# Optimization experiments

Measured on AMD Instinct MI355X. Metric: run time of the kernel, lower is better.

Reference implementation:

```python
import jax, jax.numpy as jnp
import numpy as np

B, N, D = 4, 4096, 512
E, H, TOPK = 4, 2048, 1
V_MAX, FEAT_CLAMP = 3.0, 10.0


def setup_inputs() -> dict:
    key = jax.random.key(0)
    ks = jax.random.split(key, 8)
    g = lambda k, shape, s: (jax.random.normal(k, shape, jnp.float32) * s)
    return {
        "x": g(ks[0], (B, N, D), 1.0),
        "gate_w": g(ks[1], (D, E), 0.02), "gate_b": jnp.zeros((E,), jnp.float32),
        "w1": g(ks[2], (E, D, H), 0.02), "b1": jnp.zeros((E, H), jnp.float32),
        "w2": g(ks[3], (E, H, D), 0.02), "b2": jnp.zeros((E, D), jnp.float32),
        "v_w": g(ks[4], (D,), 0.02), "v_b": jnp.zeros((), jnp.float32),
        "out_w": g(ks[5], (2, D), 0.02), "out_b": jnp.zeros((D,), jnp.float32),
        "bk_scale": jnp.asarray(1.0, jnp.float32),
    }


def _moe_ffn(x, gate_w, gate_b, w1, b1, w2, b2):
    # Sparse MoE FFN (eval mode, no dropout): top-k routing, softmax over top-k logits.
    logits = x @ gate_w + gate_b                       # (B,N,E)
    vals, idx = jax.lax.top_k(logits, TOPK)            # (B,N,K)
    wts = jax.nn.softmax(vals, axis=-1)                # (B,N,K); == 1.0 for top_k=1
    wfull = jnp.sum(jax.nn.one_hot(idx, E, dtype=x.dtype) * wts[..., None], axis=-2)  # (B,N,E)
    h = jax.nn.gelu(jnp.einsum('bnd,edh->benh', x, w1) + b1[None, :, None, :])
    y = jnp.einsum('benh,ehd->bend', h, w2) + b2[None, :, None, :]
    return jnp.einsum('bne,bend->bnd', wfull, y)


def _tridiag_green_diag(diag, sup, sub, z):
    # Diagonal of G = (T - z I)^{-1} for tridiagonal T via stable continuant ratios:
    #   L_i = theta_i/theta_{i-1},  R_i = phi_i/phi_{i+1},  G_ii = 1/(L_i + R_i - d_i)
    d = diag.astype(jnp.complex64) - z                 # (B,N)
    s = (sub * sup).astype(jnp.complex64)              # (B,N-1)
    dT = jnp.swapaxes(d, 0, 1)                         # (N,B)
    sT = jnp.swapaxes(s, 0, 1)                         # (N-1,B)

    def step(carry, inp):
        di, si = inp
        nxt = di - si / carry
        return nxt, nxt

    _, Lrest = jax.lax.scan(step, dT[0], (dT[1:], sT))
    L = jnp.concatenate([dT[:1], Lrest], axis=0)       # (N,B)
    _, Rrest = jax.lax.scan(step, dT[-1], (dT[:-1][::-1], sT[::-1]))
    R = jnp.concatenate([dT[-1:], Rrest], axis=0)[::-1]
    G = 1.0 / (L + R - dT)                             # (N,B)
    return jnp.swapaxes(G, 0, 1)                       # (B,N)


def reference(x, gate_w, gate_b, w1, b1, w2, b2, v_w, v_b, out_w, out_b, bk_scale):
    ffn_out = _moe_ffn(x, gate_w, gate_b, w1, b1, w2, b2)        # (B,N,D)
    v = jnp.clip(ffn_out @ v_w + v_b, -V_MAX, V_MAX)             # (B,N)
    he_diag = v - 2.0                                            # h0_diag_base = -2
    ones_off = jnp.ones((x.shape[0], x.shape[1] - 1), x.dtype)   # h0 sub/super = 1
    G = _tridiag_green_diag(he_diag, ones_off, ones_off, jnp.complex64(1j))
    feats = jnp.clip(jnp.stack([G.real, G.imag], axis=-1), -FEAT_CLAMP, FEAT_CLAMP)  # (B,N,2)
    spec = feats @ out_w + out_b                                 # (B,N,D)
    return ffn_out + bk_scale * spec
```

## Files before the change

### kernel.cpp

```cpp
#include <hip/hip_runtime.h>
#include <hip/hip_bf16.h>
#include <stdint.h>

#define TOK 16384
#define NSEQ 4096
#define BATCH 4
#define Dm 512
#define Em 4
#define Hm 2048

typedef __attribute__((ext_vector_type(4))) float f32x4;
typedef __attribute__((ext_vector_type(4))) unsigned int u32x4;

__device__ __forceinline__ unsigned short f2bf(float f) {
    union { float f; uint32_t u; } v; v.f = f;
    uint32_t u = v.u;
    uint32_t r = (u + 0x7FFFu + ((u >> 16) & 1u)) >> 16;
    return (unsigned short)r;
}

struct cpx { float re, im; };
__device__ __forceinline__ cpx cmul(cpx a, cpx b) { return { a.re*b.re - a.im*b.im, a.re*b.im + a.im*b.re }; }
__device__ __forceinline__ cpx csub(cpx a, cpx b) { return { a.re - b.re, a.im - b.im }; }
__device__ __forceinline__ cpx cadd(cpx a, cpx b) { return { a.re + b.re, a.im + b.im }; }
__device__ __forceinline__ cpx cdiv(cpx a, cpx b) {
    float inv = 1.0f / (b.re*b.re + b.im*b.im);
    return { (a.re*b.re + a.im*b.im)*inv, (a.im*b.re - a.re*b.im)*inv };
}

__device__ __forceinline__ void mfma_bf16(f32x4& acc, u32x4 a, u32x4 b) {
    asm("v_mfma_f32_16x16x32_bf16 %0, %1, %2, %0" : "+v"(acc) : "v"(a), "v"(b));
}

#define GLOAD_LDS16(g, l) \
    __builtin_amdgcn_global_load_lds((const __attribute__((address_space(1))) unsigned int*)(g), \
                                     (__attribute__((address_space(3))) unsigned int*)(l), 16, 0, 0)

__global__ __launch_bounds__(256) void gate_kernel(
    const float* __restrict__ x, const float* __restrict__ gate_w, const float* __restrict__ gate_b,
    unsigned short* __restrict__ xbf, int* __restrict__ expert_id)
{
    int wid = threadIdx.x >> 6, lane = threadIdx.x & 63;
    int t0 = (blockIdx.x * 4 + wid) * 8;

    const float4* gw4 = (const float4*)gate_w;
    float4 g[8];
#pragma unroll
    for (int j = 0; j < 8; j++) g[j] = gw4[lane * 8 + j];
    double gb0 = (double)gate_b[0], gb1 = (double)gate_b[1];
    double gb2 = (double)gate_b[2], gb3 = (double)gate_b[3];

    for (int tt = 0; tt < 8; tt++) {
        int t = t0 + tt;
        const float4* x4 = (const float4*)(x + (size_t)t * Dm);
        float4 xa = x4[lane * 2], xb = x4[lane * 2 + 1];

        uint4 pk;
        pk.x = (uint32_t)f2bf(xa.x) | ((uint32_t)f2bf(xa.y) << 16);
        pk.y = (uint32_t)f2bf(xa.z) | ((uint32_t)f2bf(xa.w) << 16);
        pk.z = (uint32_t)f2bf(xb.x) | ((uint32_t)f2bf(xb.y) << 16);
        pk.w = (uint32_t)f2bf(xb.z) | ((uint32_t)f2bf(xb.w) << 16);
        *(uint4*)(xbf + (size_t)t * Dm + lane * 8) = pk;

        float xv[8] = { xa.x, xa.y, xa.z, xa.w, xb.x, xb.y, xb.z, xb.w };
        double s0 = 0, s1 = 0, s2 = 0, s3 = 0;
#pragma unroll
        for (int j = 0; j < 8; j++) {
            s0 += (double)xv[j] * (double)g[j].x;
            s1 += (double)xv[j] * (double)g[j].y;
            s2 += (double)xv[j] * (double)g[j].z;
            s3 += (double)xv[j] * (double)g[j].w;
        }
#pragma unroll
        for (int off = 1; off < 64; off <<= 1) {
            s0 += __shfl_xor(s0, off);
            s1 += __shfl_xor(s1, off);
            s2 += __shfl_xor(s2, off);
            s3 += __shfl_xor(s3, off);
        }
        if (lane == 0) {
            double l0 = s0 + gb0, l1 = s1 + gb1, l2 = s2 + gb2, l3 = s3 + gb3;
            int e = 0; double best = l0;
            if (l1 > best) { best = l1; e = 1; }
            if (l2 > best) { best = l2; e = 2; }
            if (l3 > best) { best = l3; e = 3; }
            expert_id[t] = e;
        }
    }
}

__global__ __launch_bounds__(256) void transpose_cvt(
    const float* __restrict__ w1, const float* __restrict__ w2,
    unsigned short* __restrict__ w1t, unsigned short* __restrict__ w2t)
{
    int z = blockIdx.z;
    const float* src; unsigned short* dst; int R, C;
    if (z < 4) { src = w1 + (size_t)z * Dm * Hm; dst = w1t + (size_t)z * Hm * Dm; R = Dm; C = Hm; }
    else       { src = w2 + (size_t)(z - 4) * Hm * Dm; dst = w2t + (size_t)(z - 4) * Dm * Hm; R = Hm; C = Dm; }
    int c0 = blockIdx.x * 32, r0 = blockIdx.y * 32;
    if (c0 >= C || r0 >= R) return;
    __shared__ float tile[32][33];
    int tx = threadIdx.x & 31, ty = threadIdx.x >> 5;
#pragma unroll
    for (int i = 0; i < 4; i++)
        tile[ty + i * 8][tx] = src[(size_t)(r0 + ty + i * 8) * C + c0 + tx];
    __syncthreads();
#pragma unroll
    for (int i = 0; i < 4; i++)
        dst[(size_t)(c0 + ty + i * 8) * R + r0 + tx] = f2bf(tile[tx][ty + i * 8]);
}

__global__ __launch_bounds__(1024) void route_kernel(
    const int* __restrict__ expert_id, int* __restrict__ counts,
    int* __restrict__ offsets, int* __restrict__ rowmap)
{
    __shared__ int wcnt[16][4];
    __shared__ int woff[16][4];
    int wid = threadIdx.x >> 6, lane = threadIdx.x & 63;
    int base = wid * 1024;

    int myeid[16], myrank[16];
    int run0 = 0, run1 = 0, run2 = 0, run3 = 0;
#pragma unroll
    for (int s = 0; s < 16; s++) {
        int e = expert_id[base + s * 64 + lane];
        myeid[s] = e;
        unsigned long long b0 = __ballot(e & 1);
        unsigned long long b1 = __ballot(e & 2);
        unsigned long long m0 = (e & 1) ? b0 : ~b0;
        unsigned long long m1 = (e & 2) ? b1 : ~b1;
        unsigned long long same = m0 & m1;
        unsigned long long below = same & ((1ull << lane) - 1ull);
        int runh = (e == 0) ? run0 : (e == 1) ? run1 : (e == 2) ? run2 : run3;
        myrank[s] = runh + (int)__popcll(below);
        run0 += (int)__popcll(~b0 & ~b1);
        run1 += (int)__popcll(b0 & ~b1);
        run2 += (int)__popcll(~b0 & b1);
        run3 += (int)__popcll(b0 & b1);
    }
    if (lane == 0) {
        wcnt[wid][0] = run0; wcnt[wid][1] = run1; wcnt[wid][2] = run2; wcnt[wid][3] = run3;
    }
    __syncthreads();
    if (threadIdx.x == 0) {
        int t0 = 0, t1 = 0, t2 = 0, t3 = 0;
        for (int w = 0; w < 16; w++) {
            woff[w][0] = t0; woff[w][1] = t1; woff[w][2] = t2; woff[w][3] = t3;
            t0 += wcnt[w][0]; t1 += wcnt[w][1]; t2 += wcnt[w][2]; t3 += wcnt[w][3];
        }
        counts[0] = t0; counts[1] = t1; counts[2] = t2; counts[3] = t3;
        int o0 = 0, o1 = t0, o2 = t0 + t1, o3 = t0 + t1 + t2;
        offsets[0] = o0; offsets[1] = o1; offsets[2] = o2; offsets[3] = o3;
        for (int w = 0; w < 16; w++) {
            woff[w][0] += o0; woff[w][1] += o1; woff[w][2] += o2; woff[w][3] += o3;
        }
    }
    __syncthreads();
#pragma unroll
    for (int s = 0; s < 16; s++) {
        int e = myeid[s];
        rowmap[woff[wid][e] + myrank[s]] = base + s * 64 + lane;
    }
}

template<int KTOT, int NTOT, bool GATHER_A, bool GELU_EPI>
__global__ __launch_bounds__(256) void gemm_kernel(
    const unsigned short* __restrict__ A, const unsigned short* __restrict__ B,
    const float* __restrict__ bias,
    const int* __restrict__ counts, const int* __restrict__ offsets,
    const int* __restrict__ rowmap,
    unsigned short* __restrict__ Hout, float* __restrict__ Cout,
    const float* __restrict__ v_w, float* __restrict__ vpart)
{
    constexpr int NT = KTOT / 32;
    int e = blockIdx.z;
    int Me = counts[e];
    int mblk = blockIdx.y;
    if (mblk * 128 >= Me) return;
    int base = offsets[e];
    int nblk = blockIdx.x;
    int t = threadIdx.x, wid = t >> 6, lane = t & 63;

    __shared__ __align__(16) unsigned short As[3][128 * 32];
    __shared__ __align__(16) unsigned short Bs[3][128 * 32];

    const unsigned short* agp[2];
    const unsigned short* bgp[2];
#pragma unroll
    for (int c = 0; c < 2; c++) {
        int r = (c * 4 + wid) * 16 + (lane >> 2);
        int g = (lane & 3) ^ ((r >> 1) & 3);
        int mr = mblk * 128 + r; if (mr >= Me) mr = Me - 1;
        int arow = GATHER_A ? rowmap[base + mr] : (base + mr);
        agp[c] = A + (size_t)arow * KTOT + g * 8;
        int nr = nblk * 128 + r;
        bgp[c] = B + ((size_t)e * NTOT + nr) * (size_t)KTOT + g * 8;
    }

    int wm = wid >> 1, wn = wid & 1;
    int g = lane >> 4;
    int r0a = wm * 64 + (lane & 15);
    int r0b = wn * 64 + (lane & 15);
    int abase = r0a * 64 + ((g ^ ((r0a >> 1) & 3)) << 4);
    int bbase = r0b * 64 + ((g ^ ((r0b >> 1) & 3)) << 4);

    f32x4 acc[4][4] = {};

#define STAGE_T(bufi, kt) do { \
    _Pragma("unroll") \
    for (int c = 0; c < 2; c++) { \
        GLOAD_LDS16(agp[c] + (kt) * 32, &As[bufi][(c * 4 + wid) * 512]); \
        GLOAD_LDS16(bgp[c] + (kt) * 32, &Bs[bufi][(c * 4 + wid) * 512]); \
    } \
} while (0)

    STAGE_T(0, 0);
    STAGE_T(1, 1);
    int cur = 0;
    for (int kt = 0; kt < NT; ++kt) {
        int nb = cur + 2; if (nb >= 3) nb -= 3;
        if (kt + 2 < NT) {
            STAGE_T(nb, kt + 2);
            asm volatile("s_waitcnt vmcnt(8)" ::: "memory");
        } else if (kt + 1 < NT) {
            asm volatile("s_waitcnt vmcnt(4)" ::: "memory");
        } else {
            asm volatile("s_waitcnt vmcnt(0)" ::: "memory");
        }
        __builtin_amdgcn_s_barrier();

        const char* ab = (const char*)&As[cur][0];
        const char* bb = (const char*)&Bs[cur][0];
        u32x4 av[4], bv[4];
#pragma unroll
        for (int m = 0; m < 4; m++) av[m] = *(const u32x4*)(ab + abase + m * 1024);
#pragma unroll
        for (int n = 0; n < 4; n++) bv[n] = *(const u32x4*)(bb + bbase + n * 1024);
        __builtin_amdgcn_s_setprio(1);
#pragma unroll
        for (int m = 0; m < 4; m++)
#pragma unroll
            for (int n = 0; n < 4; n++)
                mfma_bf16(acc[m][n], av[m], bv[n]);
        __builtin_amdgcn_s_setprio(0);
        asm volatile("s_waitcnt lgkmcnt(0)" ::: "memory");
        __builtin_amdgcn_s_barrier();
        cur = (cur + 1 == 3) ? 0 : cur + 1;
    }
#undef STAGE_T

    float bb4[4], vw4[4];
#pragma unroll
    for (int n = 0; n < 4; n++) {
        int col = nblk * 128 + wn * 64 + n * 16 + (lane & 15);
        bb4[n] = bias[e * NTOT + col];
        if (!GELU_EPI) vw4[n] = v_w[col];
    }
#pragma unroll
    for (int m = 0; m < 4; m++) {
        int rbase = wm * 64 + m * 16 + ((lane >> 4) << 2);
#pragma unroll
        for (int j = 0; j < 4; j++) {
            int row = mblk * 128 + rbase + j;
            bool ok = row < Me;
            float p = 0.0f;
            int tok = 0;
            if (!GELU_EPI) tok = rowmap[base + (ok ? row : 0)];
#pragma unroll
            for (int n = 0; n < 4; n++) {
                int col = nblk * 128 + wn * 64 + n * 16 + (lane & 15);
                float v = acc[m][n][j] + bb4[n];
                if (GELU_EPI) {
                    if (ok) {
                        float u = 0.7978845608f * (v + 0.044715f * v * v * v);
                        float ex = __expf(2.0f * u);
                        float th = 1.0f - 2.0f / (ex + 1.0f);
                        float hv = 0.5f * v * (1.0f + th);
                        Hout[(size_t)(base + row) * NTOT + col] = f2bf(hv);
                    }
                } else {
                    if (ok) Cout[(size_t)tok * Dm + col] = v;
                    p += v * vw4[n];
                }
            }
            if (!GELU_EPI) {
                p += __shfl_xor(p, 1); p += __shfl_xor(p, 2);
                p += __shfl_xor(p, 4); p += __shfl_xor(p, 8);
                if (ok && (lane & 15) == 0) vpart[tok * 4 + nblk] = p;
            }
        }
    }
}

__global__ __launch_bounds__(256) void vdot2_kernel(
    const float4* __restrict__ vpart, const float* __restrict__ v_b, float* __restrict__ dre)
{
    int t = blockIdx.x * 256 + threadIdx.x;
    float4 p = vpart[t];
    float v = p.x + p.y + p.z + p.w + v_b[0];
    v = fminf(fmaxf(v, -3.0f), 3.0f);
    dre[t] = v - 2.0f;
}

#define SDI(i) ((i) + ((i) >> 6))
__global__ __launch_bounds__(64) void scan_kernel(
    const float* __restrict__ dre, float2* __restrict__ Lf, float2* __restrict__ Rb)
{
    int b = blockIdx.x >> 1, dir = blockIdx.x & 1;
    int lane = threadIdx.x;
    __shared__ float sd[4096 + 64];
    const float* src = dre + b * NSEQ;
    for (int i = lane; i < NSEQ; i += 64)
        sd[SDI(i)] = src[dir ? (NSEQ - 1 - i) : i];
    __syncthreads();

    cpx m00 = {1, 0}, m01 = {0, 0}, m10 = {0, 0}, m11 = {1, 0};
    int s0i = lane * 64;
#pragma unroll 4
    for (int j = 0; j < 64; j++) {
        cpx d = { sd[SDI(s0i + j)], -1.0f };
        cpx n00 = csub(cmul(d, m00), m10);
        cpx n01 = csub(cmul(d, m01), m11);
        m10 = m00; m11 = m01; m00 = n00; m01 = n01;
        if ((j & 15) == 15) {
            float mx = fmaxf(fmaxf(fmaxf(fabsf(m00.re), fabsf(m00.im)), fmaxf(fabsf(m01.re), fabsf(m01.im))),
                             fmaxf(fmaxf(fabsf(m10.re), fabsf(m10.im)), fmaxf(fabsf(m11.re), fabsf(m11.im))));
            float r = 1.0f / mx;
            m00.re *= r; m00.im *= r; m01.re *= r; m01.im *= r;
            m10.re *= r; m10.im *= r; m11.re *= r; m11.im *= r;
        }
    }

#pragma unroll
    for (int off = 1; off < 64; off <<= 1) {
        cpx q00, q01, q10, q11;
        q00.re = __shfl_up(m00.re, off); q00.im = __shfl_up(m00.im, off);
        q01.re = __shfl_up(m01.re, off); q01.im = __shfl_up(m01.im, off);
        q10.re = __shfl_up(m10.re, off); q10.im = __shfl_up(m10.im, off);
        q11.re = __shfl_up(m11.re, off); q11.im = __shfl_up(m11.im, off);
        if (lane >= off) {
            cpx r00 = cadd(cmul(m00, q00), cmul(m01, q10));
            cpx r01 = cadd(cmul(m00, q01), cmul(m01, q11));
            cpx r10 = cadd(cmul(m10, q00), cmul(m11, q10));
            cpx r11 = cadd(cmul(m10, q01), cmul(m11, q11));
            m00 = r00; m01 = r01; m10 = r10; m11 = r11;
            float mx = fmaxf(fmaxf(fmaxf(fabsf(m00.re), fabsf(m00.im)), fmaxf(fabsf(m01.re), fabsf(m01.im))),
                             fmaxf(fmaxf(fabsf(m10.re), fabsf(m10.im)), fmaxf(fabsf(m11.re), fabsf(m11.im))));
            float r = 1.0f / mx;
            m00.re *= r; m00.im *= r; m01.re *= r; m01.im *= r;
            m10.re *= r; m10.im *= r; m11.re *= r; m11.im *= r;
        }
    }

    cpx e00, e10;
    e00.re = __shfl_up(m00.re, 1); e00.im = __shfl_up(m00.im, 1);
    e10.re = __shfl_up(m10.re, 1); e10.im = __shfl_up(m10.im, 1);
    if (lane == 0) { e00 = {1, 0}; e10 = {0, 0}; }

    float2* outp = dir ? Rb : Lf;
    cpx Linv = cdiv(e10, e00);
#pragma unroll 4
    for (int j = 0; j < 64; j++) {
        int p = s0i + j;
        cpx d = { sd[SDI(p)], -1.0f };
        cpx L = csub(d, Linv);
        int idx = dir ? (NSEQ - 1 - p) : p;
        outp[b * NSEQ + idx] = make_float2(L.re, L.im);
        float inv = 1.0f / (L.re * L.re + L.im * L.im);
        Linv.re = L.re * inv; Linv.im = -L.im * inv;
    }
}

__global__ __launch_bounds__(256) void final_kernel(
    float* __restrict__ out, const float* __restrict__ dre,
    const float2* __restrict__ Lf, const float2* __restrict__ Rb,
    const float* __restrict__ out_w, const float* __restrict__ out_b,
    const float* __restrict__ bk)
{
    int t = blockIdx.x * 2 + (threadIdx.x >> 7);
    int c = threadIdx.x & 127;
    float2 L = Lf[t], R = Rb[t];
    float dr = dre[t];
    float denr = L.x + R.x - dr;
    float deni = L.y + R.y + 1.0f;
    float inv = 1.0f / (denr * denr + deni * deni);
    float f0 = fminf(fmaxf(denr * inv, -10.0f), 10.0f);
    float f1 = fminf(fmaxf(-deni * inv, -10.0f), 10.0f);
    float bks = bk[0];
    const float4* ow0 = (const float4*)out_w;
    const float4* ow1 = (const float4*)(out_w + Dm);
    const float4* ob4 = (const float4*)out_b;
    float4* o4 = (float4*)(out + (size_t)t * Dm);
    float4 w0 = ow0[c], w1v = ow1[c], ob = ob4[c];
    float4 y = o4[c];
    y.x += bks * (f0 * w0.x + f1 * w1v.x + ob.x);
    y.y += bks * (f0 * w0.y + f1 * w1v.y + ob.y);
    y.z += bks * (f0 * w0.z + f1 * w1v.z + ob.z);
    y.w += bks * (f0 * w0.w + f1 * w1v.w + ob.w);
    o4[c] = y;
}

constexpr size_t OFF_XBF    = 0;
constexpr size_t OFF_W1T    = 16777216;
constexpr size_t OFF_W2T    = OFF_W1T + 8388608;
constexpr size_t OFF_H      = OFF_W2T + 8388608;
constexpr size_t OFF_ROWMAP = OFF_H + 67108864;
constexpr size_t OFF_EID    = OFF_ROWMAP + 65536;
constexpr size_t OFF_DRE    = OFF_EID + 65536;
constexpr size_t OFF_LF     = OFF_DRE + 65536;
constexpr size_t OFF_RB     = OFF_LF + 131072;
constexpr size_t OFF_CNT    = OFF_RB + 131072;
constexpr size_t OFF_VPART  = OFF_CNT + 64;

extern "C" void kernel_launch(void* const* d_in, const int* in_sizes, int n_in,
                              void* d_out, int out_size, void* d_ws, size_t ws_size,
                              hipStream_t stream)
{
    const float* x      = (const float*)d_in[0];
    const float* gate_w = (const float*)d_in[1];
    const float* gate_b = (const float*)d_in[2];
    const float* w1     = (const float*)d_in[3];
    const float* b1     = (const float*)d_in[4];
    const float* w2     = (const float*)d_in[5];
    const float* b2     = (const float*)d_in[6];
    const float* v_w    = (const float*)d_in[7];
    const float* v_b    = (const float*)d_in[8];
    const float* out_w  = (const float*)d_in[9];
    const float* out_b  = (const float*)d_in[10];
    const float* bk     = (const float*)d_in[11];
    float* out = (float*)d_out;
    char* ws = (char*)d_ws;

    unsigned short* xbf = (unsigned short*)(ws + OFF_XBF);
    unsigned short* w1t = (unsigned short*)(ws + OFF_W1T);
    unsigned short* w2t = (unsigned short*)(ws + OFF_W2T);
    unsigned short* hbf = (unsigned short*)(ws + OFF_H);
    int* rowmap  = (int*)(ws + OFF_ROWMAP);
    int* eid     = (int*)(ws + OFF_EID);
    float* dre   = (float*)(ws + OFF_DRE);
    float2* Lf   = (float2*)(ws + OFF_LF);
    float2* Rb   = (float2*)(ws + OFF_RB);
    int* counts  = (int*)(ws + OFF_CNT);
    int* offsets = counts + 4;
    float* vpart = (float*)(ws + OFF_VPART);

    (void)in_sizes; (void)n_in; (void)out_size; (void)ws_size;

    gate_kernel<<<TOK / 32, 256, 0, stream>>>(x, gate_w, gate_b, xbf, eid);
    transpose_cvt<<<dim3(64, 64, 8), 256, 0, stream>>>(w1, w2, w1t, w2t);
    route_kernel<<<1, 1024, 0, stream>>>(eid, counts, offsets, rowmap);

    gemm_kernel<512, 2048, true, true><<<dim3(16, 128, 4), 256, 0, stream>>>(
        xbf, w1t, b1, counts, offsets, rowmap, hbf, nullptr, nullptr, nullptr);
    gemm_kernel<2048, 512, false, false><<<dim3(4, 128, 4), 256, 0, stream>>>(
        hbf, w2t, b2, counts, offsets, rowmap, nullptr, out, v_w, vpart);

    vdot2_kernel<<<TOK / 256, 256, 0, stream>>>((const float4*)vpart, v_b, dre);
    scan_kernel<<<8, 64, 0, stream>>>(dre, Lf, Rb);
    final_kernel<<<TOK / 2, 256, 0, stream>>>(out, dre, Lf, Rb, out_w, out_b, bk);
}
```

Baseline: 199.4 us.

## Widen GEMM K-tile to 64 with double buffering and 8-way XOR swizzle

```diff
diff --git a/kernel.cpp b/kernel.cpp
--- a/kernel.cpp
+++ b/kernel.cpp
@@ -172,7 +172,7 @@
     unsigned short* __restrict__ Hout, float* __restrict__ Cout,
     const float* __restrict__ v_w, float* __restrict__ vpart)
 {
-    constexpr int NT = KTOT / 32;
+    constexpr int NT = KTOT / 64;
     int e = blockIdx.z;
     int Me = counts[e];
     int mblk = blockIdx.y;
@@ -181,49 +181,56 @@
     int nblk = blockIdx.x;
     int t = threadIdx.x, wid = t >> 6, lane = t & 63;
 
-    __shared__ __align__(16) unsigned short As[3][128 * 32];
-    __shared__ __align__(16) unsigned short Bs[3][128 * 32];
-
-    const unsigned short* agp[2];
-    const unsigned short* bgp[2];
-#pragma unroll
-    for (int c = 0; c < 2; c++) {
-        int r = (c * 4 + wid) * 16 + (lane >> 2);
-        int g = (lane & 3) ^ ((r >> 1) & 3);
+    __shared__ __align__(16) unsigned short As[2][128 * 64];
+    __shared__ __align__(16) unsigned short Bs[2][128 * 64];
+
+    const unsigned short* agp[4];
+    const unsigned short* bgp[4];
+#pragma unroll
+    for (int c = 0; c < 4; c++) {
+        int f = c * 256 + t;
+        int r = f >> 3;
+        int kb = (f & 7) ^ (r & 7);
         int mr = mblk * 128 + r; if (mr >= Me) mr = Me - 1;
         int arow = GATHER_A ? rowmap[base + mr] : (base + mr);
-        agp[c] = A + (size_t)arow * KTOT + g * 8;
+        agp[c] = A + (size_t)arow * KTOT + kb * 8;
         int nr = nblk * 128 + r;
-        bgp[c] = B + ((size_t)e * NTOT + nr) * (size_t)KTOT + g * 8;
+        bgp[c] = B + ((size_t)e * NTOT + nr) * (size_t)KTOT + kb * 8;
     }
 
     int wm = wid >> 1, wn = wid & 1;
-    int g = lane >> 4;
-    int r0a = wm * 64 + (lane & 15);
-    int r0b = wn * 64 + (lane & 15);
-    int abase = r0a * 64 + ((g ^ ((r0a >> 1) & 3)) << 4);
-    int bbase = r0b * 64 + ((g ^ ((r0b >> 1) & 3)) << 4);
+    int hi = lane >> 4;
+
+    int aoffs[4], boffs[4];
+#pragma unroll
+    for (int m = 0; m < 4; m++) {
+        int ra = wm * 64 + m * 16 + (lane & 15);
+        aoffs[m] = ra * 128 + ((hi ^ (ra & 7)) << 4);
+    }
+#pragma unroll
+    for (int n = 0; n < 4; n++) {
+        int rb = wn * 64 + n * 16 + (lane & 15);
+        boffs[n] = rb * 128 + ((hi ^ (rb & 7)) << 4);
+    }
 
     f32x4 acc[4][4] = {};
 
 #define STAGE_T(bufi, kt) do { \
+    unsigned short* asd = &As[bufi][0]; \
+    unsigned short* bsd = &Bs[bufi][0]; \
     _Pragma("unroll") \
-    for (int c = 0; c < 2; c++) { \
-        GLOAD_LDS16(agp[c] + (kt) * 32, &As[bufi][(c * 4 + wid) * 512]); \
-        GLOAD_LDS16(bgp[c] + (kt) * 32, &Bs[bufi][(c * 4 + wid) * 512]); \
+    for (int c = 0; c < 4; c++) { \
+        GLOAD_LDS16(agp[c] + (kt) * 64, asd + (c * 256 + wid * 64) * 8); \
+        GLOAD_LDS16(bgp[c] + (kt) * 64, bsd + (c * 256 + wid * 64) * 8); \
     } \
 } while (0)
 
     STAGE_T(0, 0);
-    STAGE_T(1, 1);
     int cur = 0;
     for (int kt = 0; kt < NT; ++kt) {
-        int nb = cur + 2; if (nb >= 3) nb -= 3;
-        if (kt + 2 < NT) {
-            STAGE_T(nb, kt + 2);
+        if (kt + 1 < NT) {
+            STAGE_T(cur ^ 1, kt + 1);
             asm volatile("s_waitcnt vmcnt(8)" ::: "memory");
-        } else if (kt + 1 < NT) {
-            asm volatile("s_waitcnt vmcnt(4)" ::: "memory");
         } else {
             asm volatile("s_waitcnt vmcnt(0)" ::: "memory");
         }
@@ -231,21 +238,25 @@
 
         const char* ab = (const char*)&As[cur][0];
         const char* bb = (const char*)&Bs[cur][0];
-        u32x4 av[4], bv[4];
-#pragma unroll
-        for (int m = 0; m < 4; m++) av[m] = *(const u32x4*)(ab + abase + m * 1024);
-#pragma unroll
-        for (int n = 0; n < 4; n++) bv[n] = *(const u32x4*)(bb + bbase + n * 1024);
-        __builtin_amdgcn_s_setprio(1);
-#pragma unroll
-        for (int m = 0; m < 4; m++)
-#pragma unroll
-            for (int n = 0; n < 4; n++)
-                mfma_bf16(acc[m][n], av[m], bv[n]);
-        __builtin_amdgcn_s_setprio(0);
+#pragma unroll
+        for (int ks = 0; ks < 2; ks++) {
+            int kx = ks << 6;
+            u32x4 av[4], bv[4];
+#pragma unroll
+            for (int m = 0; m < 4; m++) av[m] = *(const u32x4*)(ab + (aoffs[m] ^ kx));
+#pragma unroll
+            for (int n = 0; n < 4; n++) bv[n] = *(const u32x4*)(bb + (boffs[n] ^ kx));
+            __builtin_amdgcn_s_setprio(1);
+#pragma unroll
+            for (int m = 0; m < 4; m++)
+#pragma unroll
+                for (int n = 0; n < 4; n++)
+                    mfma_bf16(acc[m][n], av[m], bv[n]);
+            __builtin_amdgcn_s_setprio(0);
+        }
         asm volatile("s_waitcnt lgkmcnt(0)" ::: "memory");
         __builtin_amdgcn_s_barrier();
-        cur = (cur + 1 == 3) ? 0 : cur + 1;
+        cur ^= 1;
     }
 #undef STAGE_T
 
```

After: 212.4 us. 1.07x slower.
